# Performance work log

Measured on AMD Instinct MI355X. Metric: run time of the kernel, lower is better.

Reference implementation:

```python
import jax, jax.numpy as jnp
import numpy as np

B, DIM, T = 16, 128, 4096
CODEBOOK = 1024


def setup_inputs() -> dict:
    key = jax.random.key(0)
    k1, k2 = jax.random.split(key)
    x = jax.random.normal(k1, (B, DIM, T), dtype=jnp.float32)
    embed = jax.random.normal(k2, (CODEBOOK, DIM), dtype=jnp.float32) * 0.02
    return {"x": x, "embed": embed}


def reference(x, embed):
    Bq, D, Tq = x.shape
    n_codes = embed.shape[0]
    # [B, D, T] -> [B*T, D]
    x_flat = x.transpose(0, 2, 1).reshape(-1, D)
    d2 = (
        jnp.sum(x_flat * x_flat, axis=-1, keepdims=True)
        - 2.0 * (x_flat @ embed.T)
        + jnp.sum(embed * embed, axis=-1)[None, :]
    )  # [N, n_codes]
    indices = jnp.argmin(d2, axis=-1)  # [N]
    quantized = embed[indices]  # [N, D]
    # commitment_loss + codebook_loss: numerically both equal mse(x, q) in fwd
    diff = x_flat - quantized
    loss = 2.0 * jnp.mean(diff * diff)
    # straight-through value equals quantized in forward
    quantized_st = quantized.reshape(Bq, Tq, D).transpose(0, 2, 1)
    # utilization = fraction of codes used (jit-safe scatter instead of unique)
    used = jnp.zeros((n_codes,), jnp.float32).at[indices].set(1.0)
    utilization = jnp.sum(used) / n_codes
    return quantized_st, indices, loss, utilization
```

## Files before the change

kernel.cpp:

```cpp
#include <hip/hip_runtime.h>
#include <hip/hip_fp16.h>

#define B_ 16
#define D_ 128
#define T_ 4096
#define C_ 1024
#define N_ (B_*T_)
#define MARGIN 1.5e-3f
#define RB 8

typedef __attribute__((ext_vector_type(8))) __fp16 fp16x8;
typedef __attribute__((ext_vector_type(4))) float f32x4;
typedef __attribute__((ext_vector_type(4))) int i32x4;
typedef unsigned int u32;

static __device__ __forceinline__ fp16x8 as_fp16x8(i32x4 v) {
    union { i32x4 i; fp16x8 h; } u; u.i = v; return u.h;
}
static __device__ __forceinline__ u32 pack_h2(float a, float b) {
    return (u32)__half_as_ushort(__float2half(a)) |
           ((u32)__half_as_ushort(__float2half(b)) << 16);
}

__global__ __launch_bounds__(256) void vq_prep_kernel(
    const float* __restrict__ embed, float* __restrict__ e2,
    u32* __restrict__ epk_hi, u32* __restrict__ epk_lo, float* __restrict__ eT,
    float* __restrict__ used, float* __restrict__ accum, int* __restrict__ nflag)
{
    int gid = blockIdx.x * 256 + threadIdx.x;
    int c = gid >> 6, d2 = gid & 63;

    float2 v = reinterpret_cast<const float2*>(embed)[gid];
    __half h0 = __float2half(v.x), h1 = __float2half(v.y);
    float l0 = v.x - __half2float(h0), l1 = v.y - __half2float(h1);
    u32 hp = (u32)__half_as_ushort(h0) | ((u32)__half_as_ushort(h1) << 16);
    u32 lp = (u32)__half_as_ushort(__float2half(l0)) |
             ((u32)__half_as_ushort(__float2half(l1)) << 16);
    int chunk = (c >> 6) * 16 + ((c >> 4) & 3) * 4 + (d2 >> 4);
    int oi = chunk * 256 + (((d2 >> 2) & 3) * 16 + (c & 15)) * 4 + (d2 & 3);
    epk_hi[oi] = hp;
    epk_lo[oi] = lp;
    int d0 = d2 * 2;
    eT[(size_t)d0 * C_ + c]       = v.x;
    eT[(size_t)(d0 + 1) * C_ + c] = v.y;

    if (gid < C_) {
        used[gid] = 0.0f;
        const float* row = embed + (size_t)gid * D_;
        {
#pragma clang fp contract(off)
            float r[8];
#pragma unroll
            for (int j = 0; j < 8; ++j) { float vv = row[j]; r[j] = vv * vv; }
            for (int i = 8; i < D_; i += 8) {
#pragma unroll
                for (int j = 0; j < 8; ++j) { float vv = row[i + j]; r[j] = r[j] + vv * vv; }
            }
            e2[gid] = ((r[0] + r[1]) + (r[2] + r[3])) + ((r[4] + r[5]) + (r[6] + r[7]));
        }
    }
    if (gid == 0) { accum[0] = 0.0f; nflag[0] = 0; }
}

__global__ __launch_bounds__(256) __attribute__((amdgpu_waves_per_eu(4, 4)))
void vq_mfma_kernel(
    const float* __restrict__ x, const u32* __restrict__ epk_hi, const u32* __restrict__ epk_lo,
    const float* __restrict__ e2, float* __restrict__ idx_f, int* __restrict__ idx_i,
    int* __restrict__ flagged, int* __restrict__ nflag)
{
    __shared__ float mv1[4][64];
    __shared__ int   mi1[4][64];
    __shared__ float mv2[4][64];

    const int g  = blockIdx.x;
    const int b  = g >> 6;
    const int t0 = (g & 63) << 6;
    const int tid = threadIdx.x;
    const int w  = tid >> 6;
    const int l  = tid & 63;
    const int r  = l & 15;
    const int q  = l >> 4;

    i32x4 xf[4][4];
    {
        const float* xp = x + (size_t)b * ((size_t)D_ * T_) + t0 + r;
#pragma unroll
        for (int s = 0; s < 4; ++s) {
#pragma unroll
            for (int t = 0; t < 4; ++t) {
                float f[8];
#pragma unroll
                for (int j = 0; j < 8; ++j)
                    f[j] = xp[16 * s + (size_t)(32 * t + 8 * q + j) * T_];
                i32x4 pk;
                pk.x = (int)pack_h2(f[0], f[1]);
                pk.y = (int)pack_h2(f[2], f[3]);
                pk.z = (int)pack_h2(f[4], f[5]);
                pk.w = (int)pack_h2(f[6], f[7]);
                xf[s][t] = pk;
            }
        }
    }
#pragma unroll
    for (int s = 0; s < 4; ++s)
#pragma unroll
        for (int t = 0; t < 4; ++t)
            asm volatile("" : "+v"(xf[s][t]));

    float rv1[4], rv2[4];
    int   ri1[4];
#pragma unroll
    for (int s = 0; s < 4; ++s) { rv1[s] = 3.4e38f; rv2[s] = 3.4e38f; ri1[s] = 0; }

    const u32* ephi = epk_hi + w * 1024 + l * 4;
    const u32* eplo = epk_lo + w * 1024 + l * 4;
    const int cbaseq = w * 16 + 4 * q;

    for (int rnd = 0; rnd < 16; ++rnd) {
        f32x4 eev = *reinterpret_cast<const f32x4*>(e2 + rnd * 64 + cbaseq);
        f32x4 acc[4];
#pragma unroll
        for (int s = 0; s < 4; ++s) acc[s] = f32x4{0.f, 0.f, 0.f, 0.f};

        __builtin_amdgcn_s_setprio(1);
#pragma unroll
        for (int t = 0; t < 4; ++t) {
            i32x4 eh = *reinterpret_cast<const i32x4*>(ephi + t * 256);
            i32x4 el = *reinterpret_cast<const i32x4*>(eplo + t * 256);
#pragma unroll
            for (int s = 0; s < 4; ++s) {
                acc[s] = __builtin_amdgcn_mfma_f32_16x16x32_f16(as_fp16x8(eh), as_fp16x8(xf[s][t]), acc[s], 0, 0, 0);
                acc[s] = __builtin_amdgcn_mfma_f32_16x16x32_f16(as_fp16x8(el), as_fp16x8(xf[s][t]), acc[s], 0, 0, 0);
            }
        }
        __builtin_amdgcn_s_setprio(0);
        ephi += 4096; eplo += 4096;

#pragma unroll
        for (int s = 0; s < 4; ++s) {
#pragma unroll
            for (int reg = 0; reg < 4; ++reg) {
                float sc = fmaf(-2.0f, acc[s][reg], eev[reg]);
                int c = rnd * 64 + cbaseq + reg;
                if (sc < rv1[s]) { rv2[s] = rv1[s]; rv1[s] = sc; ri1[s] = c; }
                else rv2[s] = fminf(rv2[s], sc);
            }
        }
    }

#pragma unroll
    for (int s = 0; s < 4; ++s) {
        float v1 = rv1[s], v2 = rv2[s];
        int   i1 = ri1[s];
#pragma unroll
        for (int mo = 0; mo < 2; ++mo) {
            int m = 16 << mo;
            float ov1 = __shfl_xor(v1, m, 64);
            int   oi1 = __shfl_xor(i1, m, 64);
            float ov2 = __shfl_xor(v2, m, 64);
            float nv2 = fminf(fmaxf(v1, ov1), fminf(v2, ov2));
            if (ov1 < v1 || (ov1 == v1 && oi1 < i1)) { v1 = ov1; i1 = oi1; }
            v2 = nv2;
        }
        if (q == 0) { mv1[w][16 * s + r] = v1; mi1[w][16 * s + r] = i1; mv2[w][16 * s + r] = v2; }
    }
    __syncthreads();

    if (tid < 64) {
        float V1 = 3.4e38f, V2 = 3.4e38f;
        int   I1 = 0;
#pragma unroll
        for (int w2 = 0; w2 < 4; ++w2) {
            float a1 = mv1[w2][tid]; int ai = mi1[w2][tid]; float a2 = mv2[w2][tid];
            if (a1 < V1 || (a1 == V1 && ai < I1)) { V2 = fminf(V2, V1); V1 = a1; I1 = ai; }
            else V2 = fminf(V2, a1);
            V2 = fminf(V2, a2);
        }
        int n = g * 64 + tid;
        idx_i[n] = I1;
        idx_f[n] = (float)I1;
        if (V2 - V1 < MARGIN) { int pos = atomicAdd(nflag, 1); flagged[pos] = n; }
    }
}

__global__ __launch_bounds__(256) void vq_refine_kernel(
    const float* __restrict__ x, const float* __restrict__ eT,
    const float* __restrict__ e2,
    const int* __restrict__ flagged, const int* __restrict__ nflag,
    float* __restrict__ idx_f, int* __restrict__ idx_i)
{
    __shared__ float xs[RB][D_];
    __shared__ float r8s[RB][8];
    __shared__ float xxs[RB];
    __shared__ float wvv[RB][4];
    __shared__ int   wvi[RB][4];

    const int tid = threadIdx.x;
    const int wv_ = tid >> 6;
    const int l   = tid & 63;
    const int total = *nflag;

    for (int base = blockIdx.x * RB; base < total; base += gridDim.x * RB) {
        __syncthreads();
#pragma unroll
        for (int e = 0; e < RB * D_ / 256; ++e) {
            int idx = tid + e * 256;
            int k = idx >> 7, d = idx & 127;
            float v = 0.f;
            int fi = base + k;
            if (fi < total) {
                int n = flagged[fi];
                int bb = n >> 12, t = n & (T_ - 1);
                v = x[(size_t)bb * ((size_t)D_ * T_) + (size_t)d * T_ + t];
            }
            xs[k][d] = v;
        }
        __syncthreads();

        if (tid < RB * 8) {
#pragma clang fp contract(off)
            int k = tid >> 3, j = tid & 7;
            float v0 = xs[k][j];
            float rj = v0 * v0;
            for (int i = 8; i < D_; i += 8) { float v = xs[k][i + j]; rj = rj + v * v; }
            r8s[k][j] = rj;
        }
        __syncthreads();
        if (tid < RB) {
#pragma clang fp contract(off)
            xxs[tid] = ((r8s[tid][0] + r8s[tid][1]) + (r8s[tid][2] + r8s[tid][3]))
                     + ((r8s[tid][4] + r8s[tid][5]) + (r8s[tid][6] + r8s[tid][7]));
        }
        __syncthreads();

        float acc[4][RB];
#pragma unroll
        for (int k2 = 0; k2 < 4; ++k2)
#pragma unroll
            for (int k = 0; k < RB; ++k) acc[k2][k] = 0.f;

        const float* ep = eT + wv_ * 256 + l;
        for (int d = 0; d < D_; ++d) {
            const float* rowp = ep + (size_t)d * C_;
            float ev0 = rowp[0], ev1 = rowp[64], ev2 = rowp[128], ev3 = rowp[192];
#pragma unroll
            for (int k = 0; k < RB; ++k) {
                float xv = xs[k][d];
                acc[0][k] = fmaf(xv, ev0, acc[0][k]);
                acc[1][k] = fmaf(xv, ev1, acc[1][k]);
                acc[2][k] = fmaf(xv, ev2, acc[2][k]);
                acc[3][k] = fmaf(xv, ev3, acc[3][k]);
            }
        }

        float e2v[4];
#pragma unroll
        for (int k2 = 0; k2 < 4; ++k2) e2v[k2] = e2[wv_ * 256 + 64 * k2 + l];

#pragma unroll
        for (int k = 0; k < RB; ++k) {
            float xx = xxs[k];
            float best = 3.4e38f;
            int   bi = 0;
#pragma unroll
            for (int k2 = 0; k2 < 4; ++k2) {
                int c = wv_ * 256 + 64 * k2 + l;
                float s;
                {
#pragma clang fp contract(off)
                    s = (xx - 2.0f * acc[k2][k]) + e2v[k2];
                }
                if (s < best) { best = s; bi = c; }
            }
#pragma unroll
            for (int m = 1; m <= 32; m <<= 1) {
                float ov = __shfl_xor(best, m, 64);
                int   oc = __shfl_xor(bi, m, 64);
                if (ov < best || (ov == best && oc < bi)) { best = ov; bi = oc; }
            }
            if (l == 0) { wvv[k][wv_] = best; wvi[k][wv_] = bi; }
        }
        __syncthreads();
        if (tid < RB) {
            int k = tid;
            if (base + k < total) {
                float V = wvv[k][0]; int I = wvi[k][0];
#pragma unroll
                for (int w2 = 1; w2 < 4; ++w2)
                    if (wvv[k][w2] < V || (wvv[k][w2] == V && wvi[k][w2] < I)) { V = wvv[k][w2]; I = wvi[k][w2]; }
                int n = flagged[base + k];
                idx_i[n] = I;
                idx_f[n] = (float)I;
            }
        }
    }
}

__global__ __launch_bounds__(256) void vq_gather_kernel(
    const float* __restrict__ x, const float* __restrict__ embed,
    const int* __restrict__ idx_i, float* __restrict__ out_q,
    float* __restrict__ accum, float* __restrict__ used)
{
    __shared__ int sidx[64];
    __shared__ float red[256];

    const int g  = blockIdx.x;
    const int b  = g >> 6;
    const int t0 = (g & 63) << 6;
    const int tid = threadIdx.x;

    if (tid < 64) {
        int ci = idx_i[g * 64 + tid];
        sidx[tid] = ci;
        used[ci] = 1.0f;
    }
    __syncthreads();

    const float* xb = x     + (size_t)b * ((size_t)D_ * T_) + t0;
    float*       ob = out_q + (size_t)b * ((size_t)D_ * T_) + t0;

    float local = 0.f;
#pragma unroll
    for (int k = 0; k < 32; ++k) {
        int e = tid + 256 * k;
        int d = e >> 6, tt = e & 63;
        float qv = embed[(size_t)sidx[tt] * D_ + d];
        float xv = xb[(size_t)d * T_ + tt];
        ob[(size_t)d * T_ + tt] = qv;
        float df = xv - qv;
        local += df * df;
    }

    red[tid] = local;
    __syncthreads();
    for (int st = 128; st > 0; st >>= 1) {
        if (tid < st) red[tid] += red[tid + st];
        __syncthreads();
    }
    if (tid == 0) atomicAdd(accum, red[0]);
}

__global__ __launch_bounds__(256) void vq_final_kernel(
    const float* __restrict__ used, const float* __restrict__ accum,
    float* __restrict__ out_loss, float* __restrict__ out_util)
{
    __shared__ float red[256];
    int tid = threadIdx.x;
    float s = 0.f;
    for (int k = tid; k < C_; k += 256) s += used[k];
    red[tid] = s;
    __syncthreads();
    for (int st = 128; st > 0; st >>= 1) {
        if (tid < st) red[tid] += red[tid + st];
        __syncthreads();
    }
    if (tid == 0) {
        out_loss[0] = 2.0f * accum[0] / (float)((size_t)N_ * D_);
        out_util[0] = red[0] / (float)C_;
    }
}

extern "C" void kernel_launch(void* const* d_in, const int* in_sizes, int n_in,
                              void* d_out, int out_size, void* d_ws, size_t ws_size,
                              hipStream_t stream) {
    const float* x     = (const float*)d_in[0];
    const float* embed = (const float*)d_in[1];

    float* out      = (float*)d_out;
    float* out_q    = out;
    float* idx_f    = out + (size_t)B_ * D_ * T_;
    float* out_loss = idx_f + N_;
    float* out_util = out_loss + 1;

    float* ws      = (float*)d_ws;
    float* e2      = ws;
    float* used    = ws + 1024;
    int*   idx_i   = (int*)(ws + 2048);
    float* accum   = ws + 67584;
    int*   nflag   = (int*)(ws + 67585);
    int*   flagged = (int*)(ws + 67588);
    u32*   epk_hi  = (u32*)(ws + 133124);
    u32*   epk_lo  = (u32*)(ws + 198660);
    float* eT      = ws + 264196;

    vq_prep_kernel  <<<256, 256, 0, stream>>>(embed, e2, epk_hi, epk_lo, eT, used, accum, nflag);
    vq_mfma_kernel  <<<N_ / 64, 256, 0, stream>>>(x, epk_hi, epk_lo, e2, idx_f, idx_i, flagged, nflag);
    vq_refine_kernel<<<256, 256, 0, stream>>>(x, eT, e2, flagged, nflag, idx_f, idx_i);
    vq_gather_kernel<<<N_ / 64, 256, 0, stream>>>(x, embed, idx_i, out_q, accum, used);
    vq_final_kernel <<<1, 256, 0, stream>>>(used, accum, out_loss, out_util);
}
```

Baseline: 102.9 us.

## Fuse gather and loss into MFMA kernel with 128-row tiles and LDS x

The separate gather kernel is folded into the MFMA argmin kernel: after picking indices, each block writes the quantized output, marks used codes and accumulates the squared error for its rows. Rows flagged as near-ties are then patched in the refine kernel, which rewrites out_q and adds a loss delta only when the index changes. The MFMA kernel moves to 512 threads handling 128 rows per block, with x fragments staged in LDS instead of registers and the codebook packing relaid for 128-code rounds. This removes one launch and a second full pass over x, at the cost of LDS reads inside the MFMA loop and more serial work in refine.

```diff
diff --git a/kernel.cpp b/kernel.cpp
--- a/kernel.cpp
+++ b/kernel.cpp
@@ -36,7 +36,7 @@
     u32 hp = (u32)__half_as_ushort(h0) | ((u32)__half_as_ushort(h1) << 16);
     u32 lp = (u32)__half_as_ushort(__float2half(l0)) |
              ((u32)__half_as_ushort(__float2half(l1)) << 16);
-    int chunk = (c >> 6) * 16 + ((c >> 4) & 3) * 4 + (d2 >> 4);
+    int chunk = (c >> 7) * 32 + ((c >> 4) & 7) * 4 + (d2 >> 4);
     int oi = chunk * 256 + (((d2 >> 2) & 3) * 16 + (c & 15)) * 4 + (d2 & 3);
     epk_hi[oi] = hp;
     epk_lo[oi] = lp;
@@ -62,65 +62,62 @@
     if (gid == 0) { accum[0] = 0.0f; nflag[0] = 0; }
 }
 
-__global__ __launch_bounds__(256) __attribute__((amdgpu_waves_per_eu(4, 4)))
-void vq_mfma_kernel(
+__global__ __launch_bounds__(512, 4) void vq_mfma_kernel(
     const float* __restrict__ x, const u32* __restrict__ epk_hi, const u32* __restrict__ epk_lo,
-    const float* __restrict__ e2, float* __restrict__ idx_f, int* __restrict__ idx_i,
-    int* __restrict__ flagged, int* __restrict__ nflag)
+    const float* __restrict__ e2, const float* __restrict__ embed,
+    float* __restrict__ out_q, float* __restrict__ idx_f, int* __restrict__ idx_i,
+    int* __restrict__ flagged, int* __restrict__ nflag,
+    float* __restrict__ accum, float* __restrict__ used)
 {
-    __shared__ float mv1[4][64];
-    __shared__ int   mi1[4][64];
-    __shared__ float mv2[4][64];
+    __shared__ i32x4 xb_lds[2048];
+    __shared__ float mv1[8][128];
+    __shared__ float mv2[8][128];
+    __shared__ int   mi1[8][128];
+    __shared__ int   sidx[128];
+    __shared__ int   sflag[128];
+    __shared__ float red[512];
 
     const int g  = blockIdx.x;
-    const int b  = g >> 6;
-    const int t0 = (g & 63) << 6;
+    const int b  = g >> 5;
+    const int t0 = (g & 31) << 7;
     const int tid = threadIdx.x;
     const int w  = tid >> 6;
     const int l  = tid & 63;
     const int r  = l & 15;
     const int q  = l >> 4;
 
-    i32x4 xf[4][4];
     {
-        const float* xp = x + (size_t)b * ((size_t)D_ * T_) + t0 + r;
-#pragma unroll
-        for (int s = 0; s < 4; ++s) {
-#pragma unroll
-            for (int t = 0; t < 4; ++t) {
-                float f[8];
-#pragma unroll
-                for (int j = 0; j < 8; ++j)
-                    f[j] = xp[16 * s + (size_t)(32 * t + 8 * q + j) * T_];
-                i32x4 pk;
-                pk.x = (int)pack_h2(f[0], f[1]);
-                pk.y = (int)pack_h2(f[2], f[3]);
-                pk.z = (int)pack_h2(f[4], f[5]);
-                pk.w = (int)pack_h2(f[6], f[7]);
-                xf[s][t] = pk;
-            }
-        }
-    }
-#pragma unroll
-    for (int s = 0; s < 4; ++s)
-#pragma unroll
-        for (int t = 0; t < 4; ++t)
-            asm volatile("" : "+v"(xf[s][t]));
-
-    float rv1[4], rv2[4];
-    int   ri1[4];
-#pragma unroll
-    for (int s = 0; s < 4; ++s) { rv1[s] = 3.4e38f; rv2[s] = 3.4e38f; ri1[s] = 0; }
+        const float* xp = x + (size_t)b * ((size_t)D_ * T_) + t0 + 16 * w + r;
+#pragma unroll
+        for (int t = 0; t < 4; ++t) {
+            float f[8];
+#pragma unroll
+            for (int j = 0; j < 8; ++j)
+                f[j] = xp[(size_t)(32 * t + 8 * q + j) * T_];
+            i32x4 pk;
+            pk.x = (int)pack_h2(f[0], f[1]);
+            pk.y = (int)pack_h2(f[2], f[3]);
+            pk.z = (int)pack_h2(f[4], f[5]);
+            pk.w = (int)pack_h2(f[6], f[7]);
+            xb_lds[(w * 4 + t) * 64 + l] = pk;
+        }
+    }
+    __syncthreads();
+
+    float rv1[8], rv2[8];
+    int   ri1[8];
+#pragma unroll
+    for (int s = 0; s < 8; ++s) { rv1[s] = 3.4e38f; rv2[s] = 3.4e38f; ri1[s] = 0; }
 
     const u32* ephi = epk_hi + w * 1024 + l * 4;
     const u32* eplo = epk_lo + w * 1024 + l * 4;
     const int cbaseq = w * 16 + 4 * q;
 
-    for (int rnd = 0; rnd < 16; ++rnd) {
-        f32x4 eev = *reinterpret_cast<const f32x4*>(e2 + rnd * 64 + cbaseq);
-        f32x4 acc[4];
-#pragma unroll
-        for (int s = 0; s < 4; ++s) acc[s] = f32x4{0.f, 0.f, 0.f, 0.f};
+    for (int rnd = 0; rnd < 8; ++rnd) {
+        f32x4 eev = *reinterpret_cast<const f32x4*>(e2 + rnd * 128 + cbaseq);
+        f32x4 acc[8];
+#pragma unroll
+        for (int s = 0; s < 8; ++s) acc[s] = f32x4{0.f, 0.f, 0.f, 0.f};
 
         __builtin_amdgcn_s_setprio(1);
 #pragma unroll
@@ -128,20 +125,21 @@
             i32x4 eh = *reinterpret_cast<const i32x4*>(ephi + t * 256);
             i32x4 el = *reinterpret_cast<const i32x4*>(eplo + t * 256);
 #pragma unroll
-            for (int s = 0; s < 4; ++s) {
-                acc[s] = __builtin_amdgcn_mfma_f32_16x16x32_f16(as_fp16x8(eh), as_fp16x8(xf[s][t]), acc[s], 0, 0, 0);
-                acc[s] = __builtin_amdgcn_mfma_f32_16x16x32_f16(as_fp16x8(el), as_fp16x8(xf[s][t]), acc[s], 0, 0, 0);
+            for (int s = 0; s < 8; ++s) {
+                i32x4 xa = xb_lds[(s * 4 + t) * 64 + l];
+                acc[s] = __builtin_amdgcn_mfma_f32_16x16x32_f16(as_fp16x8(eh), as_fp16x8(xa), acc[s], 0, 0, 0);
+                acc[s] = __builtin_amdgcn_mfma_f32_16x16x32_f16(as_fp16x8(el), as_fp16x8(xa), acc[s], 0, 0, 0);
             }
         }
         __builtin_amdgcn_s_setprio(0);
-        ephi += 4096; eplo += 4096;
-
-#pragma unroll
-        for (int s = 0; s < 4; ++s) {
+        ephi += 8192; eplo += 8192;
+
+#pragma unroll
+        for (int s = 0; s < 8; ++s) {
 #pragma unroll
             for (int reg = 0; reg < 4; ++reg) {
                 float sc = fmaf(-2.0f, acc[s][reg], eev[reg]);
-                int c = rnd * 64 + cbaseq + reg;
+                int c = rnd * 128 + cbaseq + reg;
                 if (sc < rv1[s]) { rv2[s] = rv1[s]; rv1[s] = sc; ri1[s] = c; }
                 else rv2[s] = fminf(rv2[s], sc);
             }
@@ -149,7 +147,7 @@
     }
 
 #pragma unroll
-    for (int s = 0; s < 4; ++s) {
+    for (int s = 0; s < 8; ++s) {
         float v1 = rv1[s], v2 = rv2[s];
         int   i1 = ri1[s];
 #pragma unroll
@@ -166,34 +164,69 @@
     }
     __syncthreads();
 
-    if (tid < 64) {
+    if (tid < 128) {
         float V1 = 3.4e38f, V2 = 3.4e38f;
         int   I1 = 0;
 #pragma unroll
-        for (int w2 = 0; w2 < 4; ++w2) {
+        for (int w2 = 0; w2 < 8; ++w2) {
             float a1 = mv1[w2][tid]; int ai = mi1[w2][tid]; float a2 = mv2[w2][tid];
             if (a1 < V1 || (a1 == V1 && ai < I1)) { V2 = fminf(V2, V1); V1 = a1; I1 = ai; }
             else V2 = fminf(V2, a1);
             V2 = fminf(V2, a2);
         }
-        int n = g * 64 + tid;
+        int n = g * 128 + tid;
         idx_i[n] = I1;
         idx_f[n] = (float)I1;
-        if (V2 - V1 < MARGIN) { int pos = atomicAdd(nflag, 1); flagged[pos] = n; }
+        sidx[tid] = I1;
+        int fl = (V2 - V1 < MARGIN) ? 1 : 0;
+        sflag[tid] = fl;
+        if (fl) { int pos = atomicAdd(nflag, 1); flagged[pos] = n; }
+        else used[I1] = 1.0f;
+    }
+    __syncthreads();
+
+    {
+        const float* xbase = x     + (size_t)b * ((size_t)D_ * T_) + t0;
+        float*       obase = out_q + (size_t)b * ((size_t)D_ * T_) + t0;
+        float local = 0.f;
+#pragma unroll
+        for (int k = 0; k < 8; ++k) {
+            int e = tid + 512 * k;
+            int d4 = e >> 7, p = e & 127;
+            f32x4 qv = *reinterpret_cast<const f32x4*>(embed + (size_t)sidx[p] * D_ + 4 * d4);
+            size_t base = (size_t)(4 * d4) * T_ + p;
+#pragma unroll
+            for (int i = 0; i < 4; ++i) {
+                float xv = xbase[base + (size_t)i * T_];
+                obase[base + (size_t)i * T_] = qv[i];
+                float df = xv - qv[i];
+                local = fmaf(df, df, local);
+            }
+        }
+        red[tid] = local;
+        __syncthreads();
+        for (int st = 256; st > 0; st >>= 1) {
+            if (tid < st) red[tid] += red[tid + st];
+            __syncthreads();
+        }
+        if (tid == 0) atomicAdd(accum, red[0]);
     }
 }
 
 __global__ __launch_bounds__(256) void vq_refine_kernel(
-    const float* __restrict__ x, const float* __restrict__ eT,
+    const float* __restrict__ x, const float* __restrict__ eT, const float* __restrict__ embed,
     const float* __restrict__ e2,
     const int* __restrict__ flagged, const int* __restrict__ nflag,
-    float* __restrict__ idx_f, int* __restrict__ idx_i)
+    float* __restrict__ idx_f, int* __restrict__ idx_i,
+    float* __restrict__ out_q, float* __restrict__ accum, float* __restrict__ used)
 {
     __shared__ float xs[RB][D_];
     __shared__ float r8s[RB][8];
     __shared__ float xxs[RB];
     __shared__ float wvv[RB][4];
     __shared__ int   wvi[RB][4];
+    __shared__ int   snew[RB], schg[RB], sn_[RB], sold[RB];
+    __shared__ float red[256];
 
     const int tid = threadIdx.x;
     const int wv_ = tid >> 6;
@@ -289,55 +322,37 @@
                 for (int w2 = 1; w2 < 4; ++w2)
                     if (wvv[k][w2] < V || (wvv[k][w2] == V && wvi[k][w2] < I)) { V = wvv[k][w2]; I = wvi[k][w2]; }
                 int n = flagged[base + k];
+                int iold = idx_i[n];
                 idx_i[n] = I;
                 idx_f[n] = (float)I;
-            }
-        }
-    }
-}
-
-__global__ __launch_bounds__(256) void vq_gather_kernel(
-    const float* __restrict__ x, const float* __restrict__ embed,
-    const int* __restrict__ idx_i, float* __restrict__ out_q,
-    float* __restrict__ accum, float* __restrict__ used)
-{
-    __shared__ int sidx[64];
-    __shared__ float red[256];
-
-    const int g  = blockIdx.x;
-    const int b  = g >> 6;
-    const int t0 = (g & 63) << 6;
-    const int tid = threadIdx.x;
-
-    if (tid < 64) {
-        int ci = idx_i[g * 64 + tid];
-        sidx[tid] = ci;
-        used[ci] = 1.0f;
-    }
-    __syncthreads();
-
-    const float* xb = x     + (size_t)b * ((size_t)D_ * T_) + t0;
-    float*       ob = out_q + (size_t)b * ((size_t)D_ * T_) + t0;
-
-    float local = 0.f;
-#pragma unroll
-    for (int k = 0; k < 32; ++k) {
-        int e = tid + 256 * k;
-        int d = e >> 6, tt = e & 63;
-        float qv = embed[(size_t)sidx[tt] * D_ + d];
-        float xv = xb[(size_t)d * T_ + tt];
-        ob[(size_t)d * T_ + tt] = qv;
-        float df = xv - qv;
-        local += df * df;
-    }
-
-    red[tid] = local;
-    __syncthreads();
-    for (int st = 128; st > 0; st >>= 1) {
-        if (tid < st) red[tid] += red[tid + st];
-        __syncthreads();
-    }
-    if (tid == 0) atomicAdd(accum, red[0]);
+                used[I] = 1.0f;
+                snew[k] = I; sold[k] = iold; sn_[k] = n;
+                schg[k] = (I != iold) ? 1 : 0;
+            } else schg[k] = 0;
+        }
+        __syncthreads();
+
+        float ldelta = 0.f;
+        for (int k = 0; k < RB; ++k) {
+            if (schg[k] && tid < D_) {
+                int n2 = sn_[k];
+                int bb = n2 >> 12, t = n2 & (T_ - 1);
+                float qn = embed[(size_t)snew[k] * D_ + tid];
+                float qo = embed[(size_t)sold[k] * D_ + tid];
+                float xv = xs[k][tid];
+                out_q[(size_t)bb * ((size_t)D_ * T_) + (size_t)tid * T_ + t] = qn;
+                float dn = xv - qn, dd = xv - qo;
+                ldelta += dn * dn - dd * dd;
+            }
+        }
+        red[tid] = ldelta;
+        __syncthreads();
+        for (int st = 128; st > 0; st >>= 1) {
+            if (tid < st) red[tid] += red[tid + st];
+            __syncthreads();
+        }
+        if (tid == 0 && red[0] != 0.f) atomicAdd(accum, red[0]);
+    }
 }
 
 __global__ __launch_bounds__(256) void vq_final_kernel(
@@ -384,8 +399,9 @@
     float* eT      = ws + 264196;
 
     vq_prep_kernel  <<<256, 256, 0, stream>>>(embed, e2, epk_hi, epk_lo, eT, used, accum, nflag);
-    vq_mfma_kernel  <<<N_ / 64, 256, 0, stream>>>(x, epk_hi, epk_lo, e2, idx_f, idx_i, flagged, nflag);
-    vq_refine_kernel<<<256, 256, 0, stream>>>(x, eT, e2, flagged, nflag, idx_f, idx_i);
-    vq_gather_kernel<<<N_ / 64, 256, 0, stream>>>(x, embed, idx_i, out_q, accum, used);
+    vq_mfma_kernel  <<<512, 512, 0, stream>>>(x, epk_hi, epk_lo, e2, embed,
+                                              out_q, idx_f, idx_i, flagged, nflag, accum, used);
+    vq_refine_kernel<<<256, 256, 0, stream>>>(x, eT, embed, e2, flagged, nflag,
+                                              idx_f, idx_i, out_q, accum, used);
     vq_final_kernel <<<1, 256, 0, stream>>>(used, accum, out_loss, out_util);
 }
```

Measured after the change: 221.2 us. 2.15x slower.

## Fuse gather and loss into MFMA kernel with refine-time delta correction

Applied to the files above, without the earlier changes.

Removes the separate gather kernel. The MFMA kernel now writes the quantized output, marks used codes and accumulates squared error for its tile, reading embed rows as float4. For flagged rows whose index changes, the refine kernel rewrites the output column and adds a loss delta (new minus old squared error). This saves one launch and a second full pass over x, at the cost of extra work in the MFMA kernel and more subtle correctness logic for utilization and loss.

```diff
diff --git a/kernel.cpp b/kernel.cpp
--- a/kernel.cpp
+++ b/kernel.cpp
@@ -65,12 +65,16 @@
 __global__ __launch_bounds__(256) __attribute__((amdgpu_waves_per_eu(4, 4)))
 void vq_mfma_kernel(
     const float* __restrict__ x, const u32* __restrict__ epk_hi, const u32* __restrict__ epk_lo,
-    const float* __restrict__ e2, float* __restrict__ idx_f, int* __restrict__ idx_i,
-    int* __restrict__ flagged, int* __restrict__ nflag)
+    const float* __restrict__ e2, const float* __restrict__ embed,
+    float* __restrict__ out_q, float* __restrict__ idx_f, int* __restrict__ idx_i,
+    int* __restrict__ flagged, int* __restrict__ nflag,
+    float* __restrict__ accum, float* __restrict__ used)
 {
     __shared__ float mv1[4][64];
     __shared__ int   mi1[4][64];
     __shared__ float mv2[4][64];
+    __shared__ int   sidx[64];
+    __shared__ float red[256];
 
     const int g  = blockIdx.x;
     const int b  = g >> 6;
@@ -179,21 +183,54 @@
         int n = g * 64 + tid;
         idx_i[n] = I1;
         idx_f[n] = (float)I1;
+        sidx[tid] = I1;
         if (V2 - V1 < MARGIN) { int pos = atomicAdd(nflag, 1); flagged[pos] = n; }
+        else used[I1] = 1.0f;
+    }
+    __syncthreads();
+
+    {
+        const float* xbase = x     + (size_t)b * ((size_t)D_ * T_) + t0;
+        float*       obase = out_q + (size_t)b * ((size_t)D_ * T_) + t0;
+        float local = 0.f;
+#pragma unroll
+        for (int k = 0; k < 8; ++k) {
+            int e = tid + 256 * k;
+            int d4 = e >> 6, p = e & 63;
+            f32x4 qv = *reinterpret_cast<const f32x4*>(embed + (size_t)sidx[p] * D_ + 4 * d4);
+            size_t base = (size_t)(4 * d4) * T_ + p;
+#pragma unroll
+            for (int i = 0; i < 4; ++i) {
+                float xv = xbase[base + (size_t)i * T_];
+                obase[base + (size_t)i * T_] = qv[i];
+                float df = xv - qv[i];
+                local = fmaf(df, df, local);
+            }
+        }
+        red[tid] = local;
+        __syncthreads();
+        for (int st = 128; st > 0; st >>= 1) {
+            if (tid < st) red[tid] += red[tid + st];
+            __syncthreads();
+        }
+        if (tid == 0) atomicAdd(accum, red[0]);
     }
 }
 
 __global__ __launch_bounds__(256) void vq_refine_kernel(
-    const float* __restrict__ x, const float* __restrict__ eT,
+    const float* __restrict__ x, const float* __restrict__ eT, const float* __restrict__ embed,
     const float* __restrict__ e2,
     const int* __restrict__ flagged, const int* __restrict__ nflag,
-    float* __restrict__ idx_f, int* __restrict__ idx_i)
+    float* __restrict__ idx_f, int* __restrict__ idx_i,
+    float* __restrict__ out_q, float* __restrict__ accum, float* __restrict__ used)
 {
     __shared__ float xs[RB][D_];
     __shared__ float r8s[RB][8];
     __shared__ float xxs[RB];
     __shared__ float wvv[RB][4];
     __shared__ int   wvi[RB][4];
+    __shared__ int   snew[RB], schg[RB], sn_[RB], sold[RB];
+    __shared__ float red[256];
 
     const int tid = threadIdx.x;
     const int wv_ = tid >> 6;
@@ -289,55 +326,37 @@
                 for (int w2 = 1; w2 < 4; ++w2)
                     if (wvv[k][w2] < V || (wvv[k][w2] == V && wvi[k][w2] < I)) { V = wvv[k][w2]; I = wvi[k][w2]; }
                 int n = flagged[base + k];
+                int iold = idx_i[n];
                 idx_i[n] = I;
                 idx_f[n] = (float)I;
-            }
-        }
-    }
-}
-
-__global__ __launch_bounds__(256) void vq_gather_kernel(
-    const float* __restrict__ x, const float* __restrict__ embed,
-    const int* __restrict__ idx_i, float* __restrict__ out_q,
-    float* __restrict__ accum, float* __restrict__ used)
-{
-    __shared__ int sidx[64];
-    __shared__ float red[256];
-
-    const int g  = blockIdx.x;
-    const int b  = g >> 6;
-    const int t0 = (g & 63) << 6;
-    const int tid = threadIdx.x;
-
-    if (tid < 64) {
-        int ci = idx_i[g * 64 + tid];
-        sidx[tid] = ci;
-        used[ci] = 1.0f;
-    }
-    __syncthreads();
-
-    const float* xb = x     + (size_t)b * ((size_t)D_ * T_) + t0;
-    float*       ob = out_q + (size_t)b * ((size_t)D_ * T_) + t0;
-
-    float local = 0.f;
-#pragma unroll
-    for (int k = 0; k < 32; ++k) {
-        int e = tid + 256 * k;
-        int d = e >> 6, tt = e & 63;
-        float qv = embed[(size_t)sidx[tt] * D_ + d];
-        float xv = xb[(size_t)d * T_ + tt];
-        ob[(size_t)d * T_ + tt] = qv;
-        float df = xv - qv;
-        local += df * df;
-    }
-
-    red[tid] = local;
-    __syncthreads();
-    for (int st = 128; st > 0; st >>= 1) {
-        if (tid < st) red[tid] += red[tid + st];
-        __syncthreads();
-    }
-    if (tid == 0) atomicAdd(accum, red[0]);
+                used[I] = 1.0f;
+                snew[k] = I; sold[k] = iold; sn_[k] = n;
+                schg[k] = (I != iold) ? 1 : 0;
+            } else schg[k] = 0;
+        }
+        __syncthreads();
+
+        float ldelta = 0.f;
+        for (int k = 0; k < RB; ++k) {
+            if (schg[k] && tid < D_) {
+                int n2 = sn_[k];
+                int bb = n2 >> 12, t = n2 & (T_ - 1);
+                float qn = embed[(size_t)snew[k] * D_ + tid];
+                float qo = embed[(size_t)sold[k] * D_ + tid];
+                float xv = xs[k][tid];
+                out_q[(size_t)bb * ((size_t)D_ * T_) + (size_t)tid * T_ + t] = qn;
+                float dn = xv - qn, dd = xv - qo;
+                ldelta += dn * dn - dd * dd;
+            }
+        }
+        red[tid] = ldelta;
+        __syncthreads();
+        for (int st = 128; st > 0; st >>= 1) {
+            if (tid < st) red[tid] += red[tid + st];
+            __syncthreads();
+        }
+        if (tid == 0 && red[0] != 0.f) atomicAdd(accum, red[0]);
+    }
 }
 
 __global__ __launch_bounds__(256) void vq_final_kernel(
@@ -384,8 +403,9 @@
     float* eT      = ws + 264196;
 
     vq_prep_kernel  <<<256, 256, 0, stream>>>(embed, e2, epk_hi, epk_lo, eT, used, accum, nflag);
-    vq_mfma_kernel  <<<N_ / 64, 256, 0, stream>>>(x, epk_hi, epk_lo, e2, idx_f, idx_i, flagged, nflag);
-    vq_refine_kernel<<<256, 256, 0, stream>>>(x, eT, e2, flagged, nflag, idx_f, idx_i);
-    vq_gather_kernel<<<N_ / 64, 256, 0, stream>>>(x, embed, idx_i, out_q, accum, used);
+    vq_mfma_kernel  <<<N_ / 64, 256, 0, stream>>>(x, epk_hi, epk_lo, e2, embed,
+                                                  out_q, idx_f, idx_i, flagged, nflag, accum, used);
+    vq_refine_kernel<<<256, 256, 0, stream>>>(x, eT, embed, e2, flagged, nflag,
+                                              idx_f, idx_i, out_q, accum, used);
     vq_final_kernel <<<1, 256, 0, stream>>>(used, accum, out_loss, out_util);
 }
```

After: 119.5 us. +16.1%, slower.
